# Kernel optimization log

Hardware: AMD Instinct MI355X
Metric: run time of the kernel (lower is better)

Reference implementation:

```python
import jax, jax.numpy as jnp
import numpy as np

NUM_GROUPS = 32
EPS = 1e-6


def group_norm(x, gamma, beta):
    # x: (b, c, h, w)
    b, c, h, w = x.shape
    xg = x.reshape(b, NUM_GROUPS, c // NUM_GROUPS, h, w)
    mean = xg.mean(axis=(2, 3, 4), keepdims=True)
    var = xg.var(axis=(2, 3, 4), keepdims=True)
    xn = (xg - mean) * jax.lax.rsqrt(var + EPS)
    xn = xn.reshape(b, c, h, w)
    return xn * gamma[None, :, None, None] + beta[None, :, None, None]


def conv1x1(x, w, bias):
    # x: (b, c_in, h, w), w: (c_out, c_in) -> (b, c_out, h, w)
    return jnp.einsum('oc,bchw->bohw', w, x) + bias[None, :, None, None]


def setup_inputs() -> dict:
    key = jax.random.key(0)
    ks = jax.random.split(key, 11)
    c = 512
    x = jax.random.normal(ks[0], (4, c, 64, 64), dtype=jnp.float32)
    s = 1.0 / np.sqrt(c)
    return {
        'x': x,
        'gamma': jnp.ones((c,), jnp.float32),
        'beta': jnp.zeros((c,), jnp.float32),
        'wq': jax.random.normal(ks[1], (c, c), jnp.float32) * s,
        'bq': jax.random.normal(ks[2], (c,), jnp.float32) * 0.01,
        'wk': jax.random.normal(ks[3], (c, c), jnp.float32) * s,
        'bk': jax.random.normal(ks[4], (c,), jnp.float32) * 0.01,
        'wv': jax.random.normal(ks[5], (c, c), jnp.float32) * s,
        'bv': jax.random.normal(ks[6], (c,), jnp.float32) * s,
        'wo': jax.random.normal(ks[7], (c, c), jnp.float32) * s,
        'bo': jax.random.normal(ks[8], (c,), jnp.float32) * 0.01,
    }


def reference(x, gamma, beta, wq, bq, wk, bk, wv, bv, wo, bo):
    b, c, h, w = x.shape
    scale = c ** (-0.5)
    xn = group_norm(x, gamma, beta)
    q = conv1x1(xn, wq, bq).reshape(b, c, h * w)
    k = conv1x1(xn, wk, bk).reshape(b, c, h * w)
    v = conv1x1(xn, wv, bv).reshape(b, c, h * w)
    attn = jnp.einsum('bci,bcj->bij', q, k) * scale  # (b, hw, hw)
    attn = jax.nn.softmax(attn, axis=2)
    out = jnp.einsum('bij,bcj->bci', attn, v).reshape(b, c, h, w)
    out = conv1x1(out, wo, bo)
    return x + out
```

## Files before the change

kernel.cpp:

```cpp
#include <hip/hip_runtime.h>

typedef _Float16 f16x8 __attribute__((ext_vector_type(8)));
typedef float f32x4 __attribute__((ext_vector_type(4)));
typedef unsigned short u16;
typedef unsigned short u16x8 __attribute__((ext_vector_type(8)));

__device__ __forceinline__ u16 f2h(float f) {
  union { _Float16 h; u16 u; } v; v.h = (_Float16)f; return v.u;
}
__device__ __forceinline__ float h2f(u16 u) {
  union { _Float16 h; u16 u; } v; v.u = u; return (float)v.h;
}

__device__ __forceinline__ void gload16(const u16* g, u16* l) {
  __builtin_amdgcn_global_load_lds((const __attribute__((address_space(1))) unsigned*)g,
                                   (__attribute__((address_space(3))) unsigned*)l, 16, 0, 0);
}

__global__ void rsum_k(const float* __restrict__ part, float* __restrict__ rowsum) {
  int idx = blockIdx.x * 256 + threadIdx.x;
  int bz = idx >> 12, m = idx & 4095;
  float s = 0.f;
  #pragma unroll
  for (int k = 0; k < 64; ++k)
    s += part[(size_t)(bz * 64 + k) * 4096 + m];
  rowsum[(size_t)bz * 4096 + m] = s;
}

__global__ void cast4_k(const float* __restrict__ a0, const float* __restrict__ a1,
                        const float* __restrict__ a2, const float* __restrict__ a3,
                        u16* __restrict__ o) {
  const float* src = blockIdx.y == 0 ? a0 : blockIdx.y == 1 ? a1 : blockIdx.y == 2 ? a2 : a3;
  int i = blockIdx.x * 256 + threadIdx.x;
  o[(size_t)blockIdx.y * 262144 + i] = f2h(src[i]);
}

__global__ void gn_k(const float* __restrict__ x, const float* __restrict__ g_,
                     const float* __restrict__ b_, u16* __restrict__ xnt) {
  const int g = blockIdx.x, b = blockIdx.y;
  const float* xb = x + ((size_t)b * 512 + g * 16) * 4096;
  u16* ob = xnt + (size_t)b * 4096 * 512 + g * 16;
  const float4* x4 = (const float4*)xb;
  float s = 0.f, ss = 0.f;
  for (int i = threadIdx.x; i < 16384; i += 256) {
    float4 v = x4[i];
    s += v.x + v.y + v.z + v.w;
    ss += v.x * v.x + v.y * v.y + v.z * v.z + v.w * v.w;
  }
  #pragma unroll
  for (int o = 32; o; o >>= 1) { s += __shfl_down(s, o); ss += __shfl_down(ss, o); }
  __shared__ float rs[4], rss[4];
  if ((threadIdx.x & 63) == 0) { rs[threadIdx.x >> 6] = s; rss[threadIdx.x >> 6] = ss; }
  __syncthreads();
  s = rs[0] + rs[1] + rs[2] + rs[3];
  ss = rss[0] + rss[1] + rss[2] + rss[3];
  const float mean = s * (1.f / 65536.f);
  const float rstd = rsqrtf(ss * (1.f / 65536.f) - mean * mean + 1e-6f);
  __shared__ float tile[16 * 257];
  const int cc_w = threadIdx.x & 15;
  const float gam = g_[g * 16 + cc_w] * rstd;
  const float bet = b_[g * 16 + cc_w] - mean * gam;
  for (int s0 = 0; s0 < 4096; s0 += 256) {
    __syncthreads();
    #pragma unroll
    for (int cc = 0; cc < 16; ++cc)
      tile[cc * 257 + threadIdx.x] = xb[(size_t)cc * 4096 + s0 + threadIdx.x];
    __syncthreads();
    #pragma unroll
    for (int it = 0; it < 16; ++it) {
      int sl = it * 16 + (threadIdx.x >> 4);
      float v = tile[cc_w * 257 + sl] * gam + bet;
      ob[(size_t)(s0 + sl) * 512 + cc_w] = f2h(v);
    }
  }
}

template<int MODE, int BM, int BN>
__global__ void gemm_k(const u16* __restrict__ A, int lda, long long sAz,
                       const u16* __restrict__ B, int ldb, long long sBz,
                       void* __restrict__ Cp_, int ldc, long long sCz,
                       int K,
                       u16* __restrict__ Cq, u16* __restrict__ Ck, u16* __restrict__ Cvv,
                       const float* __restrict__ bq, const float* __restrict__ bk,
                       const float* __restrict__ bvp) {
  const unsigned gx = gridDim.x, gy = gridDim.y;
  const unsigned lin = (blockIdx.z * gy + blockIdx.y) * gx + blockIdx.x;
  const unsigned nwg = gx * gy * gridDim.z;
  const unsigned swz = (lin & 7) * (nwg >> 3) + (lin >> 3);
  const unsigned bx = swz % gx;
  const unsigned rem = swz / gx;
  const unsigned by = rem % gy;
  const unsigned bz = rem / gy;

  constexpr int LK = 64;
  __shared__ u16 As[BM * LK];
  __shared__ u16 Bs[BN * LK];
  const int tid = threadIdx.x;
  const int m0 = by * BM;
  const int n0 = bx * BN;

  const u16* Ab;
  const u16* Bb;
  if constexpr (MODE == 5) {
    int proj = bz >> 2, b = bz & 3;
    Ab = A + (size_t)proj * 512 * 512;
    Bb = B + (size_t)b * 4096 * 512;
  } else {
    Ab = A + (size_t)bz * sAz;
    Bb = B + (size_t)bz * sBz;
  }

  constexpr int FM = BM / 32, FN = BN / 32;
  f32x4 acc[FM][FN];
  #pragma unroll
  for (int i = 0; i < FM; ++i)
    #pragma unroll
    for (int j = 0; j < FN; ++j)
      acc[i][j] = (f32x4){0.f, 0.f, 0.f, 0.f};

  const int wid = tid >> 6;
  const int lane = tid & 63;
  const int wm = (wid >> 1) * (BM / 2);
  const int wn = (wid & 1) * (BN / 2);
  const int l15 = lane & 15;
  const int lk8 = (lane >> 4) * 8;
  const int lrow = lane >> 3;
  const int lcol = (lane & 7) * 8;

  constexpr int ACH = BM / 8;
  constexpr int BCH = BN / 8;

  for (int k0 = 0; k0 < K; k0 += 64) {
    #pragma unroll
    for (int c = 0; c < ACH / 4; ++c) {
      int ch = wid * (ACH / 4) + c;
      gload16(Ab + (size_t)(m0 + ch * 8 + lrow) * lda + k0 + lcol, &As[ch * 512]);
    }
    #pragma unroll
    for (int c = 0; c < BCH / 4; ++c) {
      int ch = wid * (BCH / 4) + c;
      gload16(Bb + (size_t)(n0 + ch * 8 + lrow) * ldb + k0 + lcol, &Bs[ch * 512]);
    }
    __syncthreads();
    #pragma unroll
    for (int kk = 0; kk < 64; kk += 32) {
      f16x8 af[FM], bfr[FN];
      #pragma unroll
      for (int i = 0; i < FM; ++i)
        af[i] = *(const f16x8*)&As[(wm + i * 16 + l15) * LK + kk + lk8];
      #pragma unroll
      for (int j = 0; j < FN; ++j)
        bfr[j] = *(const f16x8*)&Bs[(wn + j * 16 + l15) * LK + kk + lk8];
      #pragma unroll
      for (int i = 0; i < FM; ++i)
        #pragma unroll
        for (int j = 0; j < FN; ++j)
          acc[i][j] = __builtin_amdgcn_mfma_f32_16x16x32_f16(af[i], bfr[j], acc[i][j], 0, 0, 0);
    }
    __syncthreads();
  }

  const int lq4 = (lane >> 4) * 4;
  if constexpr (MODE == 5) {
    int proj = bz >> 2, b = bz & 3;
    const float* bs = proj == 0 ? bq : (proj == 1 ? bk : bvp);
    u16* C = (proj == 0 ? Cq : (proj == 1 ? Ck : Cvv)) + (size_t)b * 4096 * 512;
    #pragma unroll
    for (int i = 0; i < FM; ++i) {
      int mb = m0 + wm + i * 16 + lq4;
      float b0 = bs[mb], b1 = bs[mb + 1], b2 = bs[mb + 2], b3 = bs[mb + 3];
      #pragma unroll
      for (int j = 0; j < FN; ++j) {
        int n = n0 + wn + j * 16 + l15;
        ushort4 o4;
        o4.x = f2h(acc[i][j][0] + b0); o4.y = f2h(acc[i][j][1] + b1);
        o4.z = f2h(acc[i][j][2] + b2); o4.w = f2h(acc[i][j][3] + b3);
        *(ushort4*)(C + (size_t)n * 512 + mb) = o4;
      }
    }
    return;
  }
  u16* C = (u16*)Cp_ + (size_t)bz * sCz;
  #pragma unroll
  for (int i = 0; i < FM; ++i) {
    int mb = m0 + wm + i * 16 + lq4;
    #pragma unroll
    for (int j = 0; j < FN; ++j) {
      int n = n0 + wn + j * 16 + l15;
      #pragma unroll
      for (int r = 0; r < 4; ++r)
        C[(size_t)(mb + r) * ldc + n] = f2h(acc[i][j][r]);
    }
  }
}

template<int BM, int BN, int EPI>
__global__ __launch_bounds__(512, 2)
void gemm8_k(const u16* __restrict__ A, int lda, long long sAz,
             const u16* __restrict__ B, int ldb, long long sBz,
             void* __restrict__ Cp_, int ldc, long long sCz,
             int K,
             const float* __restrict__ bias,
             const float* __restrict__ resid, long long sRz,
             float scale, float* __restrict__ rsptr) {
  const unsigned gx = gridDim.x, gy = gridDim.y;
  const unsigned lin = (blockIdx.z * gy + blockIdx.y) * gx + blockIdx.x;
  const unsigned nwg = gx * gy * gridDim.z;
  const unsigned swzb = (lin & 7) * (nwg >> 3) + (lin >> 3);
  const unsigned bx = swzb % gx;
  const unsigned rem = swzb / gx;
  const unsigned by = rem % gy;
  const unsigned bz = rem / gy;

  constexpr int ACH = BM / 64;
  constexpr int BCH = BN / 64;
  constexpr int NLD = ACH + BCH;
  constexpr int HBUF = (BM + BN) * 64;
  constexpr int EST = EPI == 0 ? BN + 8 : 2 * (BN + 4);
  constexpr int EPIN = BM * EST;
  constexpr int LDSN = 2 * HBUF > EPIN ? 2 * HBUF : EPIN;
  __shared__ u16 lds[LDSN];

  const int tid = threadIdx.x;
  const int m0 = by * BM;
  const int n0 = bx * BN;
  const u16* Ab = A + (size_t)bz * sAz + (size_t)m0 * lda;
  const u16* Bb = B + (size_t)bz * sBz + (size_t)n0 * ldb;

  int offA[ACH], offB[BCH];
  #pragma unroll
  for (int i = 0; i < ACH; ++i) {
    int ch = i * 512 + tid;
    int row = ch >> 3;
    int c16 = (ch & 7) ^ (row & 7);
    offA[i] = row * lda + c16 * 8;
  }
  #pragma unroll
  for (int i = 0; i < BCH; ++i) {
    int ch = i * 512 + tid;
    int row = ch >> 3;
    int c16 = (ch & 7) ^ (row & 7);
    offB[i] = row * ldb + c16 * 8;
  }

  const int wid = tid >> 6;
  const int lane = tid & 63;
  const int wm = (wid >> 2) * (BM / 2);
  const int wn = (wid & 3) * (BN / 4);
  const int l15 = lane & 15;
  const int lk8 = (lane >> 4) * 8;

  constexpr int FM = BM / 32;
  constexpr int FN = BN / 64;
  f32x4 acc[FM][FN];
  #pragma unroll
  for (int i = 0; i < FM; ++i)
    #pragma unroll
    for (int j = 0; j < FN; ++j)
      acc[i][j] = (f32x4){0.f, 0.f, 0.f, 0.f};

  const int NT = K >> 6;

  auto stage = [&](int t) {
    u16* dst = &lds[(t & 1) * HBUF];
    const u16* as = Ab + t * 64;
    #pragma unroll
    for (int i = 0; i < ACH; ++i)
      gload16(as + offA[i], dst + (i * 512 + tid) * 8);
    const u16* bs = Bb + t * 64;
    u16* dstB = dst + BM * 64;
    #pragma unroll
    for (int i = 0; i < BCH; ++i)
      gload16(bs + offB[i], dstB + (i * 512 + tid) * 8);
  };

  stage(0);
  stage(1);

  for (int t = 0; t < NT; ++t) {
    if (t < NT - 1)
      asm volatile("s_waitcnt vmcnt(%0)" :: "i"(NLD) : "memory");
    else
      asm volatile("s_waitcnt vmcnt(0)" ::: "memory");
    __builtin_amdgcn_s_barrier();
    __builtin_amdgcn_sched_barrier(0);

    const u16* Asp = &lds[(t & 1) * HBUF];
    const u16* Bsp = Asp + BM * 64;

    f16x8 bf[2][FN];
    #pragma unroll
    for (int k2 = 0; k2 < 2; ++k2)
      #pragma unroll
      for (int j = 0; j < FN; ++j) {
        int row = wn + j * 16 + l15;
        int col = (k2 * 32 + lk8) ^ ((row & 7) << 3);
        bf[k2][j] = *(const f16x8*)&Bsp[row * 64 + col];
      }
    #pragma unroll
    for (int q = 0; q < FM / 2; ++q) {
      f16x8 af[2][2];
      #pragma unroll
      for (int k2 = 0; k2 < 2; ++k2)
        #pragma unroll
        for (int s = 0; s < 2; ++s) {
          int row = wm + (2 * q + s) * 16 + l15;
          int col = (k2 * 32 + lk8) ^ ((row & 7) << 3);
          af[k2][s] = *(const f16x8*)&Asp[row * 64 + col];
        }
      __builtin_amdgcn_s_setprio(1);
      #pragma unroll
      for (int k2 = 0; k2 < 2; ++k2)
        #pragma unroll
        for (int s = 0; s < 2; ++s)
          #pragma unroll
          for (int j = 0; j < FN; ++j)
            acc[2 * q + s][j] =
                __builtin_amdgcn_mfma_f32_16x16x32_f16(af[k2][s], bf[k2][j], acc[2 * q + s][j], 0, 0, 0);
      __builtin_amdgcn_s_setprio(0);
    }

    asm volatile("s_waitcnt lgkmcnt(0)" ::: "memory");
    __builtin_amdgcn_sched_barrier(0);
    __builtin_amdgcn_s_barrier();
    if (t + 2 < NT) stage(t + 2);
  }

  const int lq4 = (lane >> 4) * 4;

  if constexpr (EPI == 0) {
    constexpr float L2E = 1.44269504088896f;
    float* part = rsptr + ((size_t)(bz * gx + bx) * 4 + (wid & 3)) * 4096;
    #pragma unroll
    for (int i = 0; i < FM; ++i) {
      #pragma unroll
      for (int j = 0; j < FN; ++j)
        #pragma unroll
        for (int r = 0; r < 4; ++r)
          acc[i][j][r] = fminf(__builtin_amdgcn_exp2f(acc[i][j][r] * (scale * L2E)), 60000.f);
      f32x4 rs = acc[i][0];
      #pragma unroll
      for (int j = 1; j < FN; ++j) rs += acc[i][j];
      #pragma unroll
      for (int off = 1; off < 16; off <<= 1) {
        f32x4 o;
        #pragma unroll
        for (int r = 0; r < 4; ++r) o[r] = __shfl_xor(rs[r], off);
        rs += o;
      }
      if (l15 == 0) {
        int mb = m0 + wm + i * 16 + lq4;
        float4 st; st.x = rs[0]; st.y = rs[1]; st.z = rs[2]; st.w = rs[3];
        *(float4*)&part[mb] = st;
      }
      #pragma unroll
      for (int j = 0; j < FN; ++j) {
        int cc = wn + j * 16 + l15;
        #pragma unroll
        for (int r = 0; r < 4; ++r)
          lds[(wm + i * 16 + lq4 + r) * EST + cc] = f2h(acc[i][j][r]);
      }
    }
    __syncthreads();
    u16* Sg = (u16*)Cp_ + (size_t)bz * sCz;
    const int col = (tid * 8) & (BN - 1);
    const int rw0 = (tid * 8) / BN;
    constexpr int RPS = 512 * 8 / BN;
    #pragma unroll
    for (int s = 0; s < BM / RPS; ++s) {
      int row = s * RPS + rw0;
      *(u16x8*)(Sg + (size_t)(m0 + row) * ldc + n0 + col) =
          *(const u16x8*)&lds[row * EST + col];
    }
  } else {
    constexpr int FST = BN + 4;
    float* tf = (float*)lds;
    #pragma unroll
    for (int i = 0; i < FM; ++i)
      #pragma unroll
      for (int j = 0; j < FN; ++j) {
        int cc = wn + j * 16 + l15;
        #pragma unroll
        for (int r = 0; r < 4; ++r)
          tf[(wm + i * 16 + lq4 + r) * FST + cc] = acc[i][j][r];
      }
    __syncthreads();
    float* C = (float*)Cp_ + (size_t)bz * sCz;
    const float* R = resid + (size_t)bz * sRz;
    const int col = (tid * 4) & (BN - 1);
    const int rw0 = (tid * 4) / BN;
    constexpr int RPS = 512 * 4 / BN;
    float4 rv = *(const float4*)&rsptr[(size_t)bz * 4096 + n0 + col];
    float4 ri;
    ri.x = 1.f / rv.x; ri.y = 1.f / rv.y; ri.z = 1.f / rv.z; ri.w = 1.f / rv.w;
    #pragma unroll
    for (int s = 0; s < BM / RPS; ++s) {
      int row = s * RPS + rw0;
      float b = bias[m0 + row];
      float4 v = *(const float4*)&tf[row * FST + col];
      float4 xr = *(const float4*)(R + (size_t)(m0 + row) * ldc + n0 + col);
      v.x = v.x * ri.x + b + xr.x;
      v.y = v.y * ri.y + b + xr.y;
      v.z = v.z * ri.z + b + xr.z;
      v.w = v.w * ri.w + b + xr.w;
      *(float4*)(C + (size_t)(m0 + row) * ldc + n0 + col) = v;
    }
  }
}

extern "C" void kernel_launch(void* const* d_in, const int* in_sizes, int n_in,
                              void* d_out, int out_size, void* d_ws, size_t ws_size,
                              hipStream_t stream) {
  const float* x     = (const float*)d_in[0];
  const float* gamma = (const float*)d_in[1];
  const float* beta  = (const float*)d_in[2];
  const float* wq    = (const float*)d_in[3];
  const float* bq    = (const float*)d_in[4];
  const float* wk    = (const float*)d_in[5];
  const float* bk    = (const float*)d_in[6];
  const float* wv    = (const float*)d_in[7];
  const float* bv    = (const float*)d_in[8];
  const float* wo    = (const float*)d_in[9];
  const float* bo    = (const float*)d_in[10];
  float* out = (float*)d_out;

  const size_t BHW = (size_t)4096 * 512;
  const long long SS = 16777216LL;
  u16* Wh  = (u16*)d_ws;
  u16* xnt = Wh + (size_t)4 * 512 * 512;
  u16* qt  = xnt + 4 * BHW;
  u16* kt  = qt + 4 * BHW;
  u16* vt  = kt + 4 * BHW;
  u16* Sb  = vt + 4 * BHW;
  float* rowsum = (float*)(Sb + 4 * SS);
  float* rspart = rowsum + 4 * 4096;
  u16* Vp  = xnt;

  const float scale = 0.044194173824159216f;

  hipLaunchKernelGGL(cast4_k, dim3(1024, 4), dim3(256), 0, stream, wq, wk, wv, wo, Wh);
  hipLaunchKernelGGL(gn_k, dim3(32, 4), dim3(256), 0, stream, x, gamma, beta, xnt);

  hipLaunchKernelGGL((gemm_k<5, 128, 128>), dim3(32, 4, 12), dim3(256), 0, stream,
                     Wh, 512, 0LL, xnt, 512, 0LL, nullptr, 0, 0LL, 512,
                     qt, kt, vt, bq, bk, bv);

  hipLaunchKernelGGL((gemm8_k<256, 256, 0>), dim3(16, 16, 4), dim3(512), 0, stream,
                     qt, 512, (long long)BHW, kt, 512, (long long)BHW,
                     Sb, 4096, SS, 512, nullptr, nullptr, 0LL, scale, rspart);

  hipLaunchKernelGGL(rsum_k, dim3(64), dim3(256), 0, stream, rspart, rowsum);

  hipLaunchKernelGGL((gemm_k<4, 128, 128>), dim3(32, 4, 4), dim3(256), 0, stream,
                     Wh + (size_t)3 * 512 * 512, 512, 0LL, vt, 512, (long long)BHW,
                     Vp, 4096, (long long)(512 * 4096), 512,
                     nullptr, nullptr, nullptr, nullptr, nullptr, nullptr);

  hipLaunchKernelGGL((gemm8_k<128, 256, 1>), dim3(16, 4, 4), dim3(512), 0, stream,
                     Vp, 4096, (long long)(512 * 4096), Sb, 4096, SS,
                     out, 4096, (long long)BHW, 4096, bo, x, (long long)BHW, 0.f, rowsum);
}
```

Measured before the change: 410.1 us.

## Split GroupNorm into stats and apply kernels, stage GEMM epilogues through LDS

```diff
diff --git a/kernel.cpp b/kernel.cpp
--- a/kernel.cpp
+++ b/kernel.cpp
@@ -7,9 +7,6 @@
 
 __device__ __forceinline__ u16 f2h(float f) {
   union { _Float16 h; u16 u; } v; v.h = (_Float16)f; return v.u;
-}
-__device__ __forceinline__ float h2f(u16 u) {
-  union { _Float16 h; u16 u; } v; v.u = u; return (float)v.h;
 }
 
 __device__ __forceinline__ void gload16(const u16* g, u16* l) {
@@ -35,12 +32,9 @@
   o[(size_t)blockIdx.y * 262144 + i] = f2h(src[i]);
 }
 
-__global__ void gn_k(const float* __restrict__ x, const float* __restrict__ g_,
-                     const float* __restrict__ b_, u16* __restrict__ xnt) {
+__global__ void gnstat_k(const float* __restrict__ x, float* __restrict__ st) {
   const int g = blockIdx.x, b = blockIdx.y;
-  const float* xb = x + ((size_t)b * 512 + g * 16) * 4096;
-  u16* ob = xnt + (size_t)b * 4096 * 512 + g * 16;
-  const float4* x4 = (const float4*)xb;
+  const float4* x4 = (const float4*)(x + ((size_t)b * 512 + g * 16) * 4096);
   float s = 0.f, ss = 0.f;
   for (int i = threadIdx.x; i < 16384; i += 256) {
     float4 v = x4[i];
@@ -52,15 +46,29 @@
   __shared__ float rs[4], rss[4];
   if ((threadIdx.x & 63) == 0) { rs[threadIdx.x >> 6] = s; rss[threadIdx.x >> 6] = ss; }
   __syncthreads();
-  s = rs[0] + rs[1] + rs[2] + rs[3];
-  ss = rss[0] + rss[1] + rss[2] + rss[3];
-  const float mean = s * (1.f / 65536.f);
-  const float rstd = rsqrtf(ss * (1.f / 65536.f) - mean * mean + 1e-6f);
+  if (threadIdx.x == 0) {
+    s = rs[0] + rs[1] + rs[2] + rs[3];
+    ss = rss[0] + rss[1] + rss[2] + rss[3];
+    const float mean = s * (1.f / 65536.f);
+    const float rstd = rsqrtf(ss * (1.f / 65536.f) - mean * mean + 1e-6f);
+    st[(b * 32 + g) * 2] = mean;
+    st[(b * 32 + g) * 2 + 1] = rstd;
+  }
+}
+
+__global__ void gnapply_k(const float* __restrict__ x, const float* __restrict__ g_,
+                          const float* __restrict__ b_, const float* __restrict__ st,
+                          u16* __restrict__ xnt) {
+  const int g = blockIdx.x, b = blockIdx.y, sc = blockIdx.z;
+  const float* xb = x + ((size_t)b * 512 + g * 16) * 4096;
+  u16* ob = xnt + (size_t)b * 4096 * 512 + g * 16;
+  const float mean = st[(b * 32 + g) * 2];
+  const float rstd = st[(b * 32 + g) * 2 + 1];
   __shared__ float tile[16 * 257];
   const int cc_w = threadIdx.x & 15;
   const float gam = g_[g * 16 + cc_w] * rstd;
   const float bet = b_[g * 16 + cc_w] - mean * gam;
-  for (int s0 = 0; s0 < 4096; s0 += 256) {
+  for (int s0 = sc * 512; s0 < sc * 512 + 512; s0 += 256) {
     __syncthreads();
     #pragma unroll
     for (int cc = 0; cc < 16; ++cc)
@@ -93,8 +101,12 @@
   const unsigned bz = rem / gy;
 
   constexpr int LK = 64;
-  __shared__ u16 As[BM * LK];
-  __shared__ u16 Bs[BN * LK];
+  constexpr int STG = (BM + BN) * LK;
+  constexpr int EPT = BN * (BM + 8) > BM * (BN + 8) ? BN * (BM + 8) : BM * (BN + 8);
+  constexpr int LDSN = STG > EPT ? STG : EPT;
+  __shared__ u16 sh[LDSN];
+  u16* As = sh;
+  u16* Bs = sh + BM * LK;
   const int tid = threadIdx.x;
   const int m0 = by * BM;
   const int n0 = bx * BN;
@@ -161,35 +173,56 @@
   }
 
   const int lq4 = (lane >> 4) * 4;
+  const int er0 = tid >> 4;
+  const int ec0 = (tid & 15) * 8;
+
   if constexpr (MODE == 5) {
     int proj = bz >> 2, b = bz & 3;
     const float* bs = proj == 0 ? bq : (proj == 1 ? bk : bvp);
+    constexpr int TS = BM + 8;
+    #pragma unroll
+    for (int i = 0; i < FM; ++i) {
+      int mbl = wm + i * 16 + lq4;
+      float b0 = bs[m0 + mbl], b1 = bs[m0 + mbl + 1],
+            b2 = bs[m0 + mbl + 2], b3 = bs[m0 + mbl + 3];
+      #pragma unroll
+      for (int j = 0; j < FN; ++j) {
+        int nl = wn + j * 16 + l15;
+        sh[nl * TS + mbl]     = f2h(acc[i][j][0] + b0);
+        sh[nl * TS + mbl + 1] = f2h(acc[i][j][1] + b1);
+        sh[nl * TS + mbl + 2] = f2h(acc[i][j][2] + b2);
+        sh[nl * TS + mbl + 3] = f2h(acc[i][j][3] + b3);
+      }
+    }
+    __syncthreads();
     u16* C = (proj == 0 ? Cq : (proj == 1 ? Ck : Cvv)) + (size_t)b * 4096 * 512;
     #pragma unroll
+    for (int s = 0; s < BN / 16; ++s) {
+      int row = s * 16 + er0;
+      *(u16x8*)(C + (size_t)(n0 + row) * 512 + m0 + ec0) = *(const u16x8*)&sh[row * TS + ec0];
+    }
+    return;
+  }
+  {
+    constexpr int TS = BN + 8;
+    #pragma unroll
     for (int i = 0; i < FM; ++i) {
-      int mb = m0 + wm + i * 16 + lq4;
-      float b0 = bs[mb], b1 = bs[mb + 1], b2 = bs[mb + 2], b3 = bs[mb + 3];
+      int mbl = wm + i * 16 + lq4;
       #pragma unroll
       for (int j = 0; j < FN; ++j) {
-        int n = n0 + wn + j * 16 + l15;
-        ushort4 o4;
-        o4.x = f2h(acc[i][j][0] + b0); o4.y = f2h(acc[i][j][1] + b1);
-        o4.z = f2h(acc[i][j][2] + b2); o4.w = f2h(acc[i][j][3] + b3);
-        *(ushort4*)(C + (size_t)n * 512 + mb) = o4;
-      }
-    }
-    return;
-  }
-  u16* C = (u16*)Cp_ + (size_t)bz * sCz;
-  #pragma unroll
-  for (int i = 0; i < FM; ++i) {
-    int mb = m0 + wm + i * 16 + lq4;
-    #pragma unroll
-    for (int j = 0; j < FN; ++j) {
-      int n = n0 + wn + j * 16 + l15;
-      #pragma unroll
-      for (int r = 0; r < 4; ++r)
-        C[(size_t)(mb + r) * ldc + n] = f2h(acc[i][j][r]);
+        int nl = wn + j * 16 + l15;
+        sh[(mbl) * TS + nl]     = f2h(acc[i][j][0]);
+        sh[(mbl + 1) * TS + nl] = f2h(acc[i][j][1]);
+        sh[(mbl + 2) * TS + nl] = f2h(acc[i][j][2]);
+        sh[(mbl + 3) * TS + nl] = f2h(acc[i][j][3]);
+      }
+    }
+    __syncthreads();
+    u16* C = (u16*)Cp_ + (size_t)bz * sCz;
+    #pragma unroll
+    for (int s = 0; s < BM / 16; ++s) {
+      int row = s * 16 + er0;
+      *(u16x8*)(C + (size_t)(m0 + row) * ldc + n0 + ec0) = *(const u16x8*)&sh[row * TS + ec0];
     }
   }
 }
@@ -207,10 +240,12 @@
   const unsigned lin = (blockIdx.z * gy + blockIdx.y) * gx + blockIdx.x;
   const unsigned nwg = gx * gy * gridDim.z;
   const unsigned swzb = (lin & 7) * (nwg >> 3) + (lin >> 3);
-  const unsigned bx = swzb % gx;
-  const unsigned rem = swzb / gx;
-  const unsigned by = rem % gy;
-  const unsigned bz = rem / gy;
+  unsigned bx, by, bz;
+  if constexpr (EPI == 1) {
+    by = swzb % gy; unsigned r2 = swzb / gy; bx = r2 % gx; bz = r2 / gx;
+  } else {
+    bx = swzb % gx; unsigned r2 = swzb / gx; by = r2 % gy; bz = r2 / gy;
+  }
 
   constexpr int ACH = BM / 64;
   constexpr int BCH = BN / 64;
@@ -434,12 +469,14 @@
   u16* Sb  = vt + 4 * BHW;
   float* rowsum = (float*)(Sb + 4 * SS);
   float* rspart = rowsum + 4 * 4096;
+  float* gstat  = rspart + (size_t)4 * 64 * 4096;
   u16* Vp  = xnt;
 
   const float scale = 0.044194173824159216f;
 
   hipLaunchKernelGGL(cast4_k, dim3(1024, 4), dim3(256), 0, stream, wq, wk, wv, wo, Wh);
-  hipLaunchKernelGGL(gn_k, dim3(32, 4), dim3(256), 0, stream, x, gamma, beta, xnt);
+  hipLaunchKernelGGL(gnstat_k, dim3(32, 4), dim3(256), 0, stream, x, gstat);
+  hipLaunchKernelGGL(gnapply_k, dim3(32, 4, 8), dim3(256), 0, stream, x, gamma, beta, gstat, xnt);
 
   hipLaunchKernelGGL((gemm_k<5, 128, 128>), dim3(32, 4, 12), dim3(256), 0, stream,
                      Wh, 512, 0LL, xnt, 512, 0LL, nullptr, 0, 0LL, 512,
```

Result: faster. 397.2 us (-3.1%).
